# Optimization experiments

Measured on AMD Instinct MI355X. Metric: run time of the kernel, lower is better.

The kernel has to match this reference:

```python
import jax, jax.numpy as jnp
import numpy as np
import math

# Fixed representative draw of the host-side RNG (all aug probs fired).
MIRROR_X, MIRROR_Y = -1.0, 1.0      # x flip on, y flip off
TX, TY = 0.06, -0.04                # translate percents
SX, SY = 1.1, 0.95                  # anisotropic scale
ZOOM = 0.9                          # isotropic zoom (draws from params['scale'] range in source)
ROT = math.radians(27.0)            # rotate degrees -> rad
SHX, SHY = 0.05, -0.03              # shear percents


def _affine_grid(theta, H, W):
    # torch F.affine_grid with align_corners=False: pixel-center normalized coords
    xs = (jnp.arange(W, dtype=jnp.float32) + 0.5) * (2.0 / W) - 1.0
    ys = (jnp.arange(H, dtype=jnp.float32) + 0.5) * (2.0 / H) - 1.0
    gx, gy = jnp.meshgrid(xs, ys)  # [H,W]
    coords = jnp.stack([gx, gy, jnp.ones_like(gx)], axis=-1)  # [H,W,3]
    return jnp.einsum('ij,hwj->hwi', theta, coords)  # [H,W,2] (x,y); same grid for all batch


def _gather(img, iy, ix, valid):
    # img [B,C,H,W]; iy/ix [H,W] int32; valid [H,W] bool. zeros padding.
    B, C, H, W = img.shape
    idx = (jnp.clip(iy, 0, H - 1) * W + jnp.clip(ix, 0, W - 1)).reshape(-1)
    g = img.reshape(B, C, H * W)[:, :, idx].reshape(B, C, H, W)
    return jnp.where(valid[None, None], g, jnp.zeros((), img.dtype))


def _unnormalize(grid, H, W):
    # align_corners=False unnormalization
    ix = ((grid[..., 0] + 1.0) * W - 1.0) * 0.5
    iy = ((grid[..., 1] + 1.0) * H - 1.0) * 0.5
    return ix, iy


def _grid_sample_bilinear(img, grid):
    B, C, H, W = img.shape
    ix, iy = _unnormalize(grid, H, W)
    x0 = jnp.floor(ix); y0 = jnp.floor(iy)
    wx1 = ix - x0; wx0 = 1.0 - wx1
    wy1 = iy - y0; wy0 = 1.0 - wy1
    x0i = x0.astype(jnp.int32); y0i = y0.astype(jnp.int32)
    x1i = x0i + 1; y1i = y0i + 1
    inb = lambda x, y: (x >= 0) & (x < W) & (y >= 0) & (y < H)
    v00 = _gather(img, y0i, x0i, inb(x0i, y0i))
    v01 = _gather(img, y0i, x1i, inb(x1i, y0i))
    v10 = _gather(img, y1i, x0i, inb(x0i, y1i))
    v11 = _gather(img, y1i, x1i, inb(x1i, y1i))
    out = (v00 * (wy0 * wx0)[None, None] + v01 * (wy0 * wx1)[None, None]
           + v10 * (wy1 * wx0)[None, None] + v11 * (wy1 * wx1)[None, None])
    return out


def _grid_sample_nearest(img, grid):
    B, C, H, W = img.shape
    ix, iy = _unnormalize(grid, H, W)
    xi = jnp.round(ix).astype(jnp.int32)
    yi = jnp.round(iy).astype(jnp.int32)
    valid = (xi >= 0) & (xi < W) & (yi >= 0) & (yi < H)
    return _gather(img, yi, xi, valid)


def _thetas():
    c, s = math.cos(ROT), math.sin(ROT)
    return [
        jnp.array([[MIRROR_X, 0.0, 0.0], [0.0, MIRROR_Y, 0.0]], jnp.float32),  # mirror
        jnp.array([[1.0, 0.0, TX], [0.0, 1.0, TY]], jnp.float32),              # translate
        jnp.array([[SX, 0.0, 0.0], [0.0, SY, 0.0]], jnp.float32),              # scale
        jnp.array([[ZOOM, 0.0, 0.0], [0.0, ZOOM, 0.0]], jnp.float32),          # zoom
        jnp.array([[c, -s, 0.0], [s, c, 0.0]], jnp.float32),                   # rotate
        jnp.array([[1.0, SHX, 0.0], [SHY, 1.0, 0.0]], jnp.float32),            # shear
    ]


def setup_inputs() -> dict:
    key = jax.random.key(0)
    k1, k2 = jax.random.split(key)
    img = jax.random.normal(k1, (16, 3, 512, 512), dtype=jnp.float32)
    label = jax.random.uniform(k2, (16, 3, 512, 512), dtype=jnp.float32)
    return {"img": img, "label": label}


def reference(img, label):
    B, C, H, W = img.shape
    # Sequential resampling, exactly as the torch module: one affine_grid +
    # grid_sample pair per enabled augmentation, bilinear for img / nearest for label.
    for theta in _thetas():
        grid = _affine_grid(theta, H, W)
        img = _grid_sample_bilinear(img, grid)
        label = _grid_sample_nearest(label, grid)
    return img, label
```

## Files before the change

kernel.cpp:

```cpp
#include <hip/hip_runtime.h>
#include <math.h>

#define HW 262144
#define TOTAL 12582912
#define TS 32
#define NT 512
#define P 2
#define NGROUP 24

#define CR 0.8910065241883679f
#define SR 0.45399049973954675f

#define K5CX (255.5f * (1.0f - CR + SR))
#define K5CY (255.5f * (1.0f - SR - CR))

#define W2 52
#define H2 44
#define W3 46
#define H3 45
#define W4 49
#define H4 48
#define W5 36
#define H5 35
#define BUFA_SZ 2352
#define BUFB_SZ 2070

struct Box { int x0, x1, y0, y1; };

__device__ __forceinline__ Box back_box(Box d, float A, float B, float C,
                                        float D, float E, float F) {
    float xa = (float)d.x0, xb = (float)d.x1, ya = (float)d.y0, yb = (float)d.y1;
    float mnx = fminf(A * xa, A * xb) + fminf(B * ya, B * yb) + C;
    float mxx = fmaxf(A * xa, A * xb) + fmaxf(B * ya, B * yb) + C;
    float mny = fminf(D * xa, D * xb) + fminf(E * ya, E * yb) + F;
    float mxy = fmaxf(D * xa, D * xb) + fmaxf(E * ya, E * yb) + F;
    Box s;
    s.x0 = (int)floorf(mnx); s.x1 = (int)floorf(mxx) + 1;
    s.y0 = (int)floorf(mny); s.y1 = (int)floorf(mxy) + 1;
    return s;
}

__device__ __forceinline__ float2 lerp2(float w, float2 a, float2 b) {
    float2 r;
    r.x = fmaf(w, b.x - a.x, a.x);
    r.y = fmaf(w, b.y - a.y, a.y);
    return r;
}

template <bool INT>
__device__ __forceinline__ void s2_eval(int i, const float* __restrict__ gin,
                                        float2* __restrict__ dst, int rx0, int ry0)
{
    int ly = i / W2;
    int lx = i - ly * W2;
    int pxi = rx0 + lx, pyi = ry0 + ly;
    if (INT) {
        int off = ((pyi - 11) << 9) + (496 - pxi);
        float2 o;
        {
            const float* g0 = gin + off;
            float h0 = fmaf(0.36f, g0[-1], 0.64f * g0[0]);
            float h1 = fmaf(0.36f, g0[511], 0.64f * g0[512]);
            o.x = fmaf(0.76f, h1, 0.24f * h0);
        }
        {
            const float* g1 = gin + HW + off;
            float h0 = fmaf(0.36f, g1[-1], 0.64f * g1[0]);
            float h1 = fmaf(0.36f, g1[511], 0.64f * g1[512]);
            o.y = fmaf(0.76f, h1, 0.24f * h0);
        }
        dst[i] = o;
    } else {
        float wx0m = ((unsigned)pxi <= 496u) ? 0.64f : 0.0f;
        float wx1m = ((unsigned)pxi <= 495u) ? 0.36f : 0.0f;
        float wy0m = ((unsigned)(pyi - 11) <= 500u) ? 0.24f : 0.0f;
        float wy1m = ((unsigned)(pyi - 10) <= 501u) ? 0.76f : 0.0f;
        int xc0 = min(max(496 - pxi, 0), 511);
        int xc1 = min(max(495 - pxi, 0), 511);
        int r0 = min(max(pyi - 11, 0), 511) << 9;
        int r1 = min(max(pyi - 10, 0), 511) << 9;
        float2 o;
        #pragma unroll
        for (int p = 0; p < P; ++p) {
            const float* g = gin + p * HW;
            float v00 = g[r0 + xc0], v01 = g[r0 + xc1];
            float v10 = g[r1 + xc0], v11 = g[r1 + xc1];
            float h0 = fmaf(wx1m, v01, wx0m * v00);
            float h1 = fmaf(wx1m, v11, wx0m * v10);
            float val = fmaf(wy1m, h1, wy0m * h0);
            if (p == 0) o.x = val; else o.y = val;
        }
        dst[i] = o;
    }
}

template <int SW, int SH, int DW, bool AXIS, bool INT>
__device__ __forceinline__ void lds_eval(int i, float A, float B, float Cs,
    float D, float E, float Fs, const float2* __restrict__ src,
    float2* __restrict__ dst, int dx0, int dy0)
{
    int ly = i / DW;
    int lx = i - ly * DW;
    int pxi = dx0 + lx, pyi = dy0 + ly;
    float px = (float)pxi, py = (float)pyi;
    float fx = AXIS ? fmaf(A, px, Cs) : fmaf(A, px, fmaf(B, py, Cs));
    float fy = AXIS ? fmaf(E, py, Fs) : fmaf(D, px, fmaf(E, py, Fs));
    float xf = floorf(fx), yf = floorf(fy);
    float wx = fx - xf, wy = fy - yf;
    int x0 = (int)xf, y0 = (int)yf;
    if (!INT) { x0 = min(max(x0, 0), SW - 2); y0 = min(max(y0, 0), SH - 2); }
    const float2* s = src + y0 * SW + x0;
    float2 v00 = s[0], v01 = s[1];
    float2 v10 = s[SW], v11 = s[SW + 1];
    float2 a0 = lerp2(wx, v00, v01);
    float2 a1 = lerp2(wx, v10, v11);
    float2 val = lerp2(wy, a0, a1);
    if (!INT) {
        if ((unsigned)pxi >= 512u || (unsigned)pyi >= 512u) { val.x = 0.f; val.y = 0.f; }
    }
    dst[i] = val;
}

template <int SW, int SH, int DW, int DTOT, bool AXIS, bool INT>
__device__ __forceinline__ void stage_lds(int tid, float A, float B, float Cs,
    float D, float E, float Fs, const float2* __restrict__ src,
    float2* __restrict__ dst, int dx0, int dy0)
{
    constexpr int FULL = DTOT / NT;
    constexpr int TAIL = DTOT - FULL * NT;
    #pragma unroll
    for (int k = 0; k < FULL; ++k)
        lds_eval<SW, SH, DW, AXIS, INT>(tid + k * NT, A, B, Cs, D, E, Fs,
                                        src, dst, dx0, dy0);
    if (TAIL && tid < TAIL)
        lds_eval<SW, SH, DW, AXIS, INT>(tid + FULL * NT, A, B, Cs, D, E, Fs,
                                        src, dst, dx0, dy0);
}

template <bool INT>
__device__ __forceinline__ void s6_eval(int ii, const float2* __restrict__ src,
    float* __restrict__ go, int tx0, int ty0, int sx0, int sy0)
{
    int lx = ii & 31, ly = ii >> 5;
    float px = (float)(tx0 + lx), py = (float)(ty0 + ly);
    float fx = fmaf(0.05f, py, -12.775f - (float)sx0) + px;
    float fy = fmaf(-0.03f, px, 7.665f - (float)sy0) + py;
    float xf = floorf(fx), yf = floorf(fy);
    float wx = fx - xf, wy = fy - yf;
    int x0 = (int)xf, y0 = (int)yf;
    if (!INT) { x0 = min(max(x0, 0), W5 - 2); y0 = min(max(y0, 0), H5 - 2); }
    const float2* s = src + y0 * W5 + x0;
    float2 v00 = s[0], v01 = s[1];
    float2 v10 = s[W5], v11 = s[W5 + 1];
    float2 a0 = lerp2(wx, v00, v01);
    float2 a1 = lerp2(wx, v10, v11);
    float2 val = lerp2(wy, a0, a1);
    int gidx = (ty0 + ly) * 512 + tx0 + lx;
    __builtin_nontemporal_store(val.x, &go[gidx]);
    __builtin_nontemporal_store(val.y, &go[HW + gidx]);
}

template <bool INT>
__device__ __forceinline__ void img_tile(int tid, const float* __restrict__ gin,
    float* __restrict__ go, int tx0, int ty0,
    Box R2, Box R3, Box R4, Box R5, float2* bufA, float2* bufB)
{
    {
        constexpr int FULL = (W2 * H2) / NT;
        constexpr int TAIL = W2 * H2 - FULL * NT;
        #pragma unroll
        for (int k = 0; k < FULL; ++k)
            s2_eval<INT>(tid + k * NT, gin, bufA, R2.x0, R2.y0);
        if (tid < TAIL) s2_eval<INT>(tid + FULL * NT, gin, bufA, R2.x0, R2.y0);
    }
    __syncthreads();
    stage_lds<W2, H2, W3, W3 * H3, true, INT>(tid,
        1.1f, 0.0f, -25.55f - (float)R2.x0,
        0.0f, 0.95f, 12.775f - (float)R2.y0, bufA, bufB, R3.x0, R3.y0);
    __syncthreads();
    stage_lds<W3, H3, W4, W4 * H4, true, INT>(tid,
        0.9f, 0.0f, 25.55f - (float)R3.x0,
        0.0f, 0.9f, 25.55f - (float)R3.y0, bufB, bufA, R4.x0, R4.y0);
    __syncthreads();
    stage_lds<W4, H4, W5, W5 * H5, false, INT>(tid,
        CR, -SR, K5CX - (float)R4.x0,
        SR,  CR, K5CY - (float)R4.y0, bufA, bufB, R5.x0, R5.y0);
    __syncthreads();
    {
        constexpr int FULL = (TS * TS) / NT;
        #pragma unroll
        for (int k = 0; k < FULL; ++k)
            s6_eval<INT>(tid + k * NT, bufB, go, tx0, ty0, R5.x0, R5.y0);
    }
}

__global__ void compose_nearest_map(int* __restrict__ map) {
    int p = blockIdx.x * blockDim.x + threadIdx.x;
    if (p >= HW) return;
    const float TH[6][6] = {
        { 1.0f,  0.05f, 0.0f,  -0.03f, 1.0f,  0.0f },
        { CR,    -SR,   0.0f,   SR,    CR,    0.0f },
        { 0.9f,  0.0f,  0.0f,   0.0f,  0.9f,  0.0f },
        { 1.1f,  0.0f,  0.0f,   0.0f,  0.95f, 0.0f },
        { 1.0f,  0.0f,  0.06f,  0.0f,  1.0f, -0.04f },
        { -1.0f, 0.0f,  0.0f,   0.0f,  1.0f,  0.0f },
    };
    int cx = p & 511, cy = p >> 9;
    bool valid = true;
    #pragma unroll
    for (int s = 0; s < 6; ++s) {
        if (!valid) break;
        float x = (cx + 0.5f) * (2.0f / 512.0f) - 1.0f;
        float y = (cy + 0.5f) * (2.0f / 512.0f) - 1.0f;
        float gx = TH[s][0] * x + TH[s][1] * y + TH[s][2];
        float gy = TH[s][3] * x + TH[s][4] * y + TH[s][5];
        float ix = ((gx + 1.0f) * 512.0f - 1.0f) * 0.5f;
        float iy = ((gy + 1.0f) * 512.0f - 1.0f) * 0.5f;
        float xr = rintf(ix), yr = rintf(iy);
        if (xr < 0.0f || xr > 511.0f || yr < 0.0f || yr > 511.0f) valid = false;
        else { cx = (int)xr; cy = (int)yr; }
    }
    map[p] = valid ? (cy * 512 + cx) : -1;
}

__global__ __launch_bounds__(NT, 8) void fused_all(
    const float* __restrict__ img, const float* __restrict__ lab,
    const int* __restrict__ map, float* __restrict__ oimg,
    float* __restrict__ olab)
{
    __shared__ float2 bufA[BUFA_SZ];
    __shared__ float2 bufB[BUFB_SZ];
    int tid = threadIdx.x;
    int b = blockIdx.x;
    int group = b >> 8, tile = b & 255;
    int tx0 = (tile & 15) * TS, ty0 = (tile >> 4) * TS;
    int pbase = group * P;
    const float* gin = img + pbase * HW;
    const float* lin = lab + pbase * HW;
    float* go = oimg + pbase * HW;
    float* lo = olab + pbase * HW;

    {
        constexpr int FULL = (TS * TS) / NT;
        #pragma unroll
        for (int k = 0; k < FULL; ++k) {
            int ii = tid + k * NT;
            int gidx = (ty0 + (ii >> 5)) * 512 + tx0 + (ii & 31);
            int m = map[gidx];
            float v0 = (m >= 0) ? lin[m] : 0.f;
            float v1 = (m >= 0) ? lin[HW + m] : 0.f;
            __builtin_nontemporal_store(v0, &lo[gidx]);
            __builtin_nontemporal_store(v1, &lo[HW + gidx]);
        }
    }

    Box R6 = {tx0, tx0 + TS - 1, ty0, ty0 + TS - 1};
    Box R5 = back_box(R6, 1.0f, 0.05f, -12.775f, -0.03f, 1.0f, 7.665f);
    R5.x1 = min(R5.x1, R5.x0 + W5 - 1); R5.y1 = min(R5.y1, R5.y0 + H5 - 1);
    Box R4 = back_box(R5, CR, -SR, K5CX, SR, CR, K5CY);
    R4.x1 = min(R4.x1, R4.x0 + W4 - 1); R4.y1 = min(R4.y1, R4.y0 + H4 - 1);
    Box R3 = back_box(R4, 0.9f, 0.0f, 25.55f, 0.0f, 0.9f, 25.55f);
    R3.x1 = min(R3.x1, R3.x0 + W3 - 1); R3.y1 = min(R3.y1, R3.y0 + H3 - 1);
    Box R2 = back_box(R3, 1.1f, 0.0f, -25.55f, 0.0f, 0.95f, 12.775f);

    bool dead = (R2.x1 < 0 || R2.x0 > 511 || R2.y1 < 0 || R2.y0 > 511)
             || (R3.x1 < 0 || R3.x0 > 511 || R3.y1 < 0 || R3.y0 > 511)
             || (R4.x1 < 0 || R4.x0 > 511 || R4.y1 < 0 || R4.y0 > 511)
             || (R5.x1 < 0 || R5.x0 > 511 || R5.y1 < 0 || R5.y0 > 511);
    if (dead) {
        constexpr int FULL = (TS * TS) / NT;
        #pragma unroll
        for (int k = 0; k < FULL; ++k) {
            int ii = tid + k * NT;
            int gidx = (ty0 + (ii >> 5)) * 512 + tx0 + (ii & 31);
            __builtin_nontemporal_store(0.f, &go[gidx]);
            __builtin_nontemporal_store(0.f, &go[HW + gidx]);
        }
        return;
    }

    bool interior =
        R2.x0 >= 0 && R2.x0 + W2 - 1 <= 495 && R2.y0 >= 11 && R2.y0 + H2 - 1 <= 511 &&
        R3.x0 >= 0 && R3.x0 + W3 - 1 <= 511 && R3.y0 >= 0 && R3.y0 + H3 - 1 <= 511 &&
        R4.x0 >= 0 && R4.x0 + W4 - 1 <= 511 && R4.y0 >= 0 && R4.y0 + H4 - 1 <= 511 &&
        R5.x0 >= 0 && R5.x0 + W5 - 1 <= 511 && R5.y0 >= 0 && R5.y0 + H5 - 1 <= 511;

    if (interior)
        img_tile<true >(tid, gin, go, tx0, ty0, R2, R3, R4, R5, bufA, bufB);
    else
        img_tile<false>(tid, gin, go, tx0, ty0, R2, R3, R4, R5, bufA, bufB);
}

extern "C" void kernel_launch(void* const* d_in, const int* in_sizes, int n_in,
                              void* d_out, int out_size, void* d_ws, size_t ws_size,
                              hipStream_t stream) {
    const float* img_in = (const float*)d_in[0];
    const float* lab_in = (const float*)d_in[1];
    float* out_img = (float*)d_out;
    float* out_lab = (float*)d_out + TOTAL;
    int* map = (int*)d_ws;

    compose_nearest_map<<<(HW + 255) / 256, 256, 0, stream>>>(map);
    fused_all<<<NGROUP * 256, NT, 0, stream>>>(img_in, lab_in, map, out_img, out_lab);
}
```

Measured before the change: 67.86 us.

## Fuse first two bilinear stages into a 3x3 global-read stencil for interior tiles

For interior tiles, the mirror+translate stage and the anisotropic scale stage are merged into one pass. Each output of stage 3 is computed directly from a 3x3 neighbourhood of global input with combined separable weights, so the 52x44 LDS intermediate, one barrier and one LDS resampling pass are removed. The cost is more global loads per stage-3 point (9 per plane instead of 4 per stage-2 point). The fused weights also round slightly differently from the sequential reference. Boundary tiles keep the original path.

Measured after the change: 71.75 us. 1.06x slower.

```diff
diff --git a/kernel.cpp b/kernel.cpp
--- a/kernel.cpp
+++ b/kernel.cpp
@@ -47,51 +47,70 @@
     return r;
 }
 
-template <bool INT>
-__device__ __forceinline__ void s2_eval(int i, const float* __restrict__ gin,
-                                        float2* __restrict__ dst, int rx0, int ry0)
+__device__ __forceinline__ void s23_eval(int i, const float* __restrict__ gin,
+                                         float2* __restrict__ dst, int r3x0, int r3y0)
+{
+    int ly = i / W3;
+    int lx = i - ly * W3;
+    float px = (float)(r3x0 + lx), py = (float)(r3y0 + ly);
+    float fx = fmaf(1.1f, px, -25.55f);
+    float fy = fmaf(0.95f, py, 12.775f);
+    float xf = floorf(fx), yf = floorf(fy);
+    float wx = fx - xf, wy = fy - yf;
+    int x0 = (int)xf, y0 = (int)yf;
+    int off = ((y0 - 11) << 9) + (496 - x0);
+    const float* g0 = gin + off;
+    const float* g1 = g0 + HW;
+    float u0 = fmaf(-0.64f, wx, 0.64f);
+    float u1 = fmaf(0.28f, wx, 0.36f);
+    float u2 = 0.36f * wx;
+    float t0 = fmaf(-0.24f, wy, 0.24f);
+    float t1 = fmaf(-0.52f, wy, 0.76f);
+    float t2 = 0.76f * wy;
+    float a0 = g0[0],    a1 = g0[-1],   a2 = g0[-2];
+    float a3 = g0[512],  a4 = g0[511],  a5 = g0[510];
+    float a6 = g0[1024], a7 = g0[1023], a8 = g0[1022];
+    float b0 = g1[0],    b1 = g1[-1],   b2 = g1[-2];
+    float b3 = g1[512],  b4 = g1[511],  b5 = g1[510];
+    float b6 = g1[1024], b7 = g1[1023], b8 = g1[1022];
+    float r0a = fmaf(u0, a0, fmaf(u1, a1, u2 * a2));
+    float r1a = fmaf(u0, a3, fmaf(u1, a4, u2 * a5));
+    float r2a = fmaf(u0, a6, fmaf(u1, a7, u2 * a8));
+    float r0b = fmaf(u0, b0, fmaf(u1, b1, u2 * b2));
+    float r1b = fmaf(u0, b3, fmaf(u1, b4, u2 * b5));
+    float r2b = fmaf(u0, b6, fmaf(u1, b7, u2 * b8));
+    float2 o;
+    o.x = fmaf(t0, r0a, fmaf(t1, r1a, t2 * r2a));
+    o.y = fmaf(t0, r0b, fmaf(t1, r1b, t2 * r2b));
+    dst[i] = o;
+}
+
+__device__ __forceinline__ void s2_eval_gen(int i, const float* __restrict__ gin,
+                                            float2* __restrict__ dst, int rx0, int ry0)
 {
     int ly = i / W2;
     int lx = i - ly * W2;
     int pxi = rx0 + lx, pyi = ry0 + ly;
-    if (INT) {
-        int off = ((pyi - 11) << 9) + (496 - pxi);
-        float2 o;
-        {
-            const float* g0 = gin + off;
-            float h0 = fmaf(0.36f, g0[-1], 0.64f * g0[0]);
-            float h1 = fmaf(0.36f, g0[511], 0.64f * g0[512]);
-            o.x = fmaf(0.76f, h1, 0.24f * h0);
-        }
-        {
-            const float* g1 = gin + HW + off;
-            float h0 = fmaf(0.36f, g1[-1], 0.64f * g1[0]);
-            float h1 = fmaf(0.36f, g1[511], 0.64f * g1[512]);
-            o.y = fmaf(0.76f, h1, 0.24f * h0);
-        }
-        dst[i] = o;
-    } else {
-        float wx0m = ((unsigned)pxi <= 496u) ? 0.64f : 0.0f;
-        float wx1m = ((unsigned)pxi <= 495u) ? 0.36f : 0.0f;
-        float wy0m = ((unsigned)(pyi - 11) <= 500u) ? 0.24f : 0.0f;
-        float wy1m = ((unsigned)(pyi - 10) <= 501u) ? 0.76f : 0.0f;
-        int xc0 = min(max(496 - pxi, 0), 511);
-        int xc1 = min(max(495 - pxi, 0), 511);
-        int r0 = min(max(pyi - 11, 0), 511) << 9;
-        int r1 = min(max(pyi - 10, 0), 511) << 9;
-        float2 o;
-        #pragma unroll
-        for (int p = 0; p < P; ++p) {
-            const float* g = gin + p * HW;
-            float v00 = g[r0 + xc0], v01 = g[r0 + xc1];
-            float v10 = g[r1 + xc0], v11 = g[r1 + xc1];
-            float h0 = fmaf(wx1m, v01, wx0m * v00);
-            float h1 = fmaf(wx1m, v11, wx0m * v10);
-            float val = fmaf(wy1m, h1, wy0m * h0);
-            if (p == 0) o.x = val; else o.y = val;
-        }
-        dst[i] = o;
-    }
+    float wx0m = ((unsigned)pxi <= 496u) ? 0.64f : 0.0f;
+    float wx1m = ((unsigned)pxi <= 495u) ? 0.36f : 0.0f;
+    float wy0m = ((unsigned)(pyi - 11) <= 500u) ? 0.24f : 0.0f;
+    float wy1m = ((unsigned)(pyi - 10) <= 501u) ? 0.76f : 0.0f;
+    int xc0 = min(max(496 - pxi, 0), 511);
+    int xc1 = min(max(495 - pxi, 0), 511);
+    int r0 = min(max(pyi - 11, 0), 511) << 9;
+    int r1 = min(max(pyi - 10, 0), 511) << 9;
+    float2 o;
+    #pragma unroll
+    for (int p = 0; p < P; ++p) {
+        const float* g = gin + p * HW;
+        float v00 = g[r0 + xc0], v01 = g[r0 + xc1];
+        float v10 = g[r1 + xc0], v11 = g[r1 + xc1];
+        float h0 = fmaf(wx1m, v01, wx0m * v00);
+        float h1 = fmaf(wx1m, v11, wx0m * v10);
+        float val = fmaf(wy1m, h1, wy0m * h0);
+        if (p == 0) o.x = val; else o.y = val;
+    }
+    dst[i] = o;
 }
 
 template <int SW, int SH, int DW, bool AXIS, bool INT>
@@ -160,8 +179,33 @@
     __builtin_nontemporal_store(val.y, &go[HW + gidx]);
 }
 
-template <bool INT>
-__device__ __forceinline__ void img_tile(int tid, const float* __restrict__ gin,
+__device__ __forceinline__ void img_tile_fast(int tid, const float* __restrict__ gin,
+    float* __restrict__ go, int tx0, int ty0, Box R3, Box R4, Box R5,
+    float2* bufA, float2* bufB)
+{
+    {
+        constexpr int FULL = (W3 * H3) / NT;
+        constexpr int TAIL = W3 * H3 - FULL * NT;
+        #pragma unroll
+        for (int k = 0; k < FULL; ++k)
+            s23_eval(tid + k * NT, gin, bufB, R3.x0, R3.y0);
+        if (tid < TAIL) s23_eval(tid + FULL * NT, gin, bufB, R3.x0, R3.y0);
+    }
+    __syncthreads();
+    stage_lds<W3, H3, W4, W4 * H4, true, true>(tid,
+        0.9f, 0.0f, 25.55f - (float)R3.x0,
+        0.0f, 0.9f, 25.55f - (float)R3.y0, bufB, bufA, R4.x0, R4.y0);
+    __syncthreads();
+    stage_lds<W4, H4, W5, W5 * H5, false, true>(tid,
+        CR, -SR, K5CX - (float)R4.x0,
+        SR,  CR, K5CY - (float)R4.y0, bufA, bufB, R5.x0, R5.y0);
+    __syncthreads();
+    #pragma unroll
+    for (int k = 0; k < (TS * TS) / NT; ++k)
+        s6_eval<true>(tid + k * NT, bufB, go, tx0, ty0, R5.x0, R5.y0);
+}
+
+__device__ __forceinline__ void img_tile_gen(int tid, const float* __restrict__ gin,
     float* __restrict__ go, int tx0, int ty0,
     Box R2, Box R3, Box R4, Box R5, float2* bufA, float2* bufB)
 {
@@ -170,28 +214,25 @@
         constexpr int TAIL = W2 * H2 - FULL * NT;
         #pragma unroll
         for (int k = 0; k < FULL; ++k)
-            s2_eval<INT>(tid + k * NT, gin, bufA, R2.x0, R2.y0);
-        if (tid < TAIL) s2_eval<INT>(tid + FULL * NT, gin, bufA, R2.x0, R2.y0);
-    }
-    __syncthreads();
-    stage_lds<W2, H2, W3, W3 * H3, true, INT>(tid,
+            s2_eval_gen(tid + k * NT, gin, bufA, R2.x0, R2.y0);
+        if (tid < TAIL) s2_eval_gen(tid + FULL * NT, gin, bufA, R2.x0, R2.y0);
+    }
+    __syncthreads();
+    stage_lds<W2, H2, W3, W3 * H3, true, false>(tid,
         1.1f, 0.0f, -25.55f - (float)R2.x0,
         0.0f, 0.95f, 12.775f - (float)R2.y0, bufA, bufB, R3.x0, R3.y0);
     __syncthreads();
-    stage_lds<W3, H3, W4, W4 * H4, true, INT>(tid,
+    stage_lds<W3, H3, W4, W4 * H4, true, false>(tid,
         0.9f, 0.0f, 25.55f - (float)R3.x0,
         0.0f, 0.9f, 25.55f - (float)R3.y0, bufB, bufA, R4.x0, R4.y0);
     __syncthreads();
-    stage_lds<W4, H4, W5, W5 * H5, false, INT>(tid,
+    stage_lds<W4, H4, W5, W5 * H5, false, false>(tid,
         CR, -SR, K5CX - (float)R4.x0,
         SR,  CR, K5CY - (float)R4.y0, bufA, bufB, R5.x0, R5.y0);
     __syncthreads();
-    {
-        constexpr int FULL = (TS * TS) / NT;
-        #pragma unroll
-        for (int k = 0; k < FULL; ++k)
-            s6_eval<INT>(tid + k * NT, bufB, go, tx0, ty0, R5.x0, R5.y0);
-    }
+    #pragma unroll
+    for (int k = 0; k < (TS * TS) / NT; ++k)
+        s6_eval<false>(tid + k * NT, bufB, go, tx0, ty0, R5.x0, R5.y0);
 }
 
 __global__ void compose_nearest_map(int* __restrict__ map) {
@@ -240,18 +281,15 @@
     float* go = oimg + pbase * HW;
     float* lo = olab + pbase * HW;
 
-    {
-        constexpr int FULL = (TS * TS) / NT;
-        #pragma unroll
-        for (int k = 0; k < FULL; ++k) {
-            int ii = tid + k * NT;
-            int gidx = (ty0 + (ii >> 5)) * 512 + tx0 + (ii & 31);
-            int m = map[gidx];
-            float v0 = (m >= 0) ? lin[m] : 0.f;
-            float v1 = (m >= 0) ? lin[HW + m] : 0.f;
-            __builtin_nontemporal_store(v0, &lo[gidx]);
-            __builtin_nontemporal_store(v1, &lo[HW + gidx]);
-        }
+    #pragma unroll
+    for (int k = 0; k < (TS * TS) / NT; ++k) {
+        int ii = tid + k * NT;
+        int gidx = (ty0 + (ii >> 5)) * 512 + tx0 + (ii & 31);
+        int m = map[gidx];
+        float v0 = (m >= 0) ? lin[m] : 0.f;
+        float v1 = (m >= 0) ? lin[HW + m] : 0.f;
+        __builtin_nontemporal_store(v0, &lo[gidx]);
+        __builtin_nontemporal_store(v1, &lo[HW + gidx]);
     }
 
     Box R6 = {tx0, tx0 + TS - 1, ty0, ty0 + TS - 1};
@@ -268,9 +306,8 @@
              || (R4.x1 < 0 || R4.x0 > 511 || R4.y1 < 0 || R4.y0 > 511)
              || (R5.x1 < 0 || R5.x0 > 511 || R5.y1 < 0 || R5.y0 > 511);
     if (dead) {
-        constexpr int FULL = (TS * TS) / NT;
         #pragma unroll
-        for (int k = 0; k < FULL; ++k) {
+        for (int k = 0; k < (TS * TS) / NT; ++k) {
             int ii = tid + k * NT;
             int gidx = (ty0 + (ii >> 5)) * 512 + tx0 + (ii & 31);
             __builtin_nontemporal_store(0.f, &go[gidx]);
@@ -286,9 +323,9 @@
         R5.x0 >= 0 && R5.x0 + W5 - 1 <= 511 && R5.y0 >= 0 && R5.y0 + H5 - 1 <= 511;
 
     if (interior)
-        img_tile<true >(tid, gin, go, tx0, ty0, R2, R3, R4, R5, bufA, bufB);
+        img_tile_fast(tid, gin, go, tx0, ty0, R3, R4, R5, bufA, bufB);
     else
-        img_tile<false>(tid, gin, go, tx0, ty0, R2, R3, R4, R5, bufA, bufB);
+        img_tile_gen(tid, gin, go, tx0, ty0, R2, R3, R4, R5, bufA, bufB);
 }
 
 extern "C" void kernel_launch(void* const* d_in, const int* in_sizes, int n_in,
```
